# Performance work log

Hardware: AMD Instinct MI355X
Metric: run time of the kernel (lower is better)

## Reference

```python
import jax, jax.numpy as jnp
import numpy as np

GAMMA = 0.99
LMBD = 0.95  # lambda is unused in live math: in-loop advantages are overwritten by returns - values
EPS = 0.2
T, S, H, A = 262144, 128, 1024, 16


def setup_inputs() -> dict:
    key = jax.random.key(0)
    ks = jax.random.split(key, 12)
    states = jax.random.normal(ks[0], (T, S), jnp.float32)
    actions = jax.random.normal(ks[1], (T, A), jnp.float32)
    rewards = jax.random.normal(ks[2], (T, 1), jnp.float32)
    values = jax.random.normal(ks[3], (T, 1), jnp.float32)
    masks = jax.random.randint(ks[4], (T, 1), 0, 2, jnp.int32)
    W1 = jax.random.normal(ks[5], (S, H), jnp.float32) / np.sqrt(S)
    b1 = jnp.zeros((H,), jnp.float32)
    W_mu = jax.random.normal(ks[6], (H, A), jnp.float32) / np.sqrt(H)
    b_mu = jnp.zeros((A,), jnp.float32)
    W_lv = jax.random.normal(ks[7], (H, A), jnp.float32) / np.sqrt(H)
    b_lv = jnp.zeros((A,), jnp.float32)
    # beta (old policy) log-probs: computed from the same net + small noise so that
    # ratio = exp(sum(pi_logp - beta_logp)) stays numerically reasonable, as in real PPO.
    h = jnp.tanh(states @ W1 + b1)
    mu = h @ W_mu + b_mu
    std = jnp.exp(0.5 * (h @ W_lv + b_lv))
    logp = -0.5 * jnp.square((actions - mu) / std) - jnp.log(std) - 0.5 * jnp.log(2.0 * jnp.pi)
    beta_log_probs = logp + 0.01 * jax.random.normal(ks[8], (T, A), jnp.float32)
    return dict(states=states, actions=actions, rewards=rewards, values=values,
                beta_log_probs=beta_log_probs, W1=W1, b1=b1, W_mu=W_mu, b_mu=b_mu,
                W_lv=W_lv, b_lv=b_lv, masks=masks)


def reference(states, actions, rewards, values, beta_log_probs,
              W1, b1, W_mu, b_mu, W_lv, b_lv, masks):
    m = masks.astype(rewards.dtype)  # [T,1] 1=continue, 0=episode boundary

    # reversed masked discounted-return recurrence: returns[i] = r[i] + gamma * prev_return * m[i]
    def step(prev_ret, inp):
        r, mi = inp
        ret = r + GAMMA * prev_ret * mi
        return ret, ret

    _, returns = jax.lax.scan(step, jnp.zeros((1,), rewards.dtype), (rewards, m), reverse=True)
    # (deltas / in-loop GAE advantages in the source are dead code: overwritten below)
    advantages = returns - values                      # [T,1]
    a_hat = (advantages - advantages.mean()) / (advantages.std(ddof=1) + 1e-7)

    # pi(states) -> mu, logvar (value head unused here)
    h = jnp.tanh(states @ W1 + b1)                     # [T,H]
    mu = h @ W_mu + b_mu                               # [T,A]
    logvar = h @ W_lv + b_lv
    std = jnp.exp(0.5 * logvar)
    pi_log_probs = -0.5 * jnp.square((actions - mu) / std) - jnp.log(std) - 0.5 * jnp.log(2.0 * jnp.pi)

    blp = jax.lax.stop_gradient(beta_log_probs)        # .detach() in source
    ratio = jnp.exp(jnp.sum(pi_log_probs - blp, axis=1, keepdims=True))  # [T,1]

    actor_loss = -jnp.mean(jnp.minimum(ratio * a_hat,
                                       jnp.clip(ratio, 1.0 - EPS, 1.0 + EPS) * a_hat))
    critic_loss = jnp.mean(jnp.square(advantages))
    return actor_loss + critic_loss
```

## Files before the change

### kernel.cpp

```cpp
#include <hip/hip_runtime.h>
#include <math.h>


typedef __attribute__((ext_vector_type(8))) short short8_t;
typedef __attribute__((ext_vector_type(4))) short short4_t;
typedef __attribute__((ext_vector_type(4))) float float4_t;
typedef __attribute__((ext_vector_type(4))) unsigned uint4_t;

#define T_TOTAL 262144
#define S_DIM 128
#define H_DIM 1024
#define A_DIM 16
#define GAMMA 0.99f
#define SEG_LEN 64
#define NSEG 4096
#define GRP 16
#define NGRP 256

#define WS_SUM   0
#define WS_SUMSQ 1
#define WS_MEAN  2
#define WS_ISTD  3
#define WS_TERM  4
#define WS_SEGA  8
#define WS_SEGB  (WS_SEGA + NSEG)
#define WS_INC   (WS_SEGB + NSEG)
#define WS_ADV   (WS_INC + NSEG)
#define WS_W1F   (WS_ADV + T_TOTAL)
#define WS_WHF   (WS_W1F + 65536)

#define SM_SIZE 32784

__device__ __forceinline__ short f2bf(float f) {
  unsigned u = __float_as_uint(f);
  u += 0x7fffu + ((u >> 16) & 1u);
  return (short)(u >> 16);
}

__device__ __forceinline__ float fast_tanh(float x) {
  float e = __expf(2.0f * x);
  return 1.0f - __fdividef(2.0f, e + 1.0f);
}

__device__ __forceinline__ unsigned cvt_pk_bf16(float lo, float hi) {
  unsigned r;
  asm("v_cvt_pk_bf16_f32 %0, %1, %2" : "=v"(r) : "v"(lo), "v"(hi));
  return r;
}

__device__ __forceinline__ void permlane32_swap2(unsigned& a, unsigned& b) {
  asm("v_permlane32_swap_b32 %0, %1" : "+v"(a), "+v"(b));
}

__global__ void prep_all(const float* __restrict__ W1,
                         const float* __restrict__ W_mu,
                         const float* __restrict__ W_lv,
                         const float* __restrict__ rewards,
                         const int* __restrict__ masks,
                         float* __restrict__ ws,
                         short* __restrict__ w1f,
                         short* __restrict__ whf) {
  const int blk = blockIdx.x;
  if (blk < 64) {
    int id = blk * 256 + threadIdx.x;
    int lane = id & 63;
    int kf = (id >> 6) & 3;
    int nt = id >> 8;
    int quad = lane >> 4, col = nt * 16 + (lane & 15);
    int kbase = kf * 32 + quad * 8;
#pragma unroll
    for (int e = 0; e < 8; ++e)
      w1f[(size_t)id * 8 + e] = f2bf(W1[(size_t)(kbase + e) * H_DIM + col]);
  } else if (blk < 80) {
    int id = (blk - 64) * 256 + threadIdx.x;
    int lane = id & 63;
    int kf = (id >> 6) & 31;
    int nt = id >> 11;
    const float* src = nt ? W_lv : W_mu;
    int quad = lane >> 4, col = lane & 15;
    int hbase = kf * 32 + ((quad >> 1) << 4) + ((quad & 1) << 2);
#pragma unroll
    for (int e = 0; e < 8; ++e) {
      int hh = hbase + ((e >> 2) << 3) + (e & 3);
      whf[(size_t)id * 8 + e] = f2bf(src[(size_t)hh * A_DIM + col]);
    }
  } else if (blk < 96) {
    int g = (blk - 80) * 256 + threadIdx.x;
    int lo = g * SEG_LEN;
    const float4* r4 = (const float4*)(rewards + lo);
    const int4* m4 = (const int4*)(masks + lo);
    float a = 1.0f, b = 0.0f;
#pragma unroll 4
    for (int c = 15; c >= 0; --c) {
      float4 r = r4[c]; int4 mm = m4[c];
      float gi;
      gi = GAMMA * (float)mm.w; b = r.w + gi * b; a = gi * a;
      gi = GAMMA * (float)mm.z; b = r.z + gi * b; a = gi * a;
      gi = GAMMA * (float)mm.y; b = r.y + gi * b; a = gi * a;
      gi = GAMMA * (float)mm.x; b = r.x + gi * b; a = gi * a;
    }
    ws[WS_SEGA + g] = a;
    ws[WS_SEGB + g] = b;
  } else {
    if (threadIdx.x < 8) ws[threadIdx.x] = 0.0f;
  }
}

__global__ void scan_pass2(float* __restrict__ ws) {
  __shared__ float gA[NGRP], gB[NGRP], ginc[NGRP];
  int t = threadIdx.x;
  int lo = t * GRP, hi = lo + GRP - 1;
  float A = 1.0f, B = 0.0f;
  for (int s = hi; s >= lo; --s) {
    float as = ws[WS_SEGA + s], bs = ws[WS_SEGB + s];
    B = bs + as * B;
    A = as * A;
  }
  gA[t] = A; gB[t] = B;
  __syncthreads();
  if (t == 0) {
    float x = 0.0f;
    ginc[NGRP - 1] = 0.0f;
    for (int g = NGRP - 1; g >= 1; --g) {
      x = gB[g] + gA[g] * x;
      ginc[g - 1] = x;
    }
  }
  __syncthreads();
  float x = ginc[t];
  for (int s = hi; s >= lo; --s) {
    ws[WS_INC + s] = x;
    x = ws[WS_SEGB + s] + ws[WS_SEGA + s] * x;
  }
}

__global__ void scan_pass3(const float* __restrict__ rewards,
                           const int* __restrict__ masks,
                           const float* __restrict__ values,
                           float* __restrict__ ws) {
  int g = blockIdx.x * blockDim.x + threadIdx.x;
  int lo = g * SEG_LEN;
  float x = ws[WS_INC + g];
  const float4* r4 = (const float4*)(rewards + lo);
  const int4* m4 = (const int4*)(masks + lo);
  const float4* v4 = (const float4*)(values + lo);
  float4* adv4 = (float4*)(ws + WS_ADV + lo);
  float s1 = 0.0f, s2 = 0.0f;
#pragma unroll 4
  for (int c = 15; c >= 0; --c) {
    float4 r = r4[c]; int4 mm = m4[c]; float4 v = v4[c];
    float gi;
    gi = GAMMA * (float)mm.w; x = r.w + gi * x; float aw = x - v.w;
    gi = GAMMA * (float)mm.z; x = r.z + gi * x; float az = x - v.z;
    gi = GAMMA * (float)mm.y; x = r.y + gi * x; float ay = x - v.y;
    gi = GAMMA * (float)mm.x; x = r.x + gi * x; float ax = x - v.x;
    float4 o; o.x = ax; o.y = ay; o.z = az; o.w = aw;
    adv4[c] = o;
    s1 += ax + ay + az + aw;
    s2 += ax * ax + ay * ay + az * az + aw * aw;
  }
  for (int m = 1; m < 64; m <<= 1) {
    s1 += __shfl_xor(s1, m);
    s2 += __shfl_xor(s2, m);
  }
  if ((threadIdx.x & 63) == 0) {
    atomicAdd(&ws[WS_SUM], s1);
    atomicAdd(&ws[WS_SUMSQ], s2);
  }
}

__launch_bounds__(256, 2)
__global__ void main2(const float* __restrict__ states,
                      const float* __restrict__ actions,
                      const float* __restrict__ beta,
                      const float* __restrict__ b1g,
                      const float* __restrict__ bmug,
                      const float* __restrict__ blvg,
                      const short* __restrict__ W1f,
                      const short* __restrict__ Whf,
                      float* __restrict__ ws) {
  __shared__ __align__(16) unsigned char smem[SM_SIZE];
  short* Ab = (short*)smem;

  const int tid = threadIdx.x;
  const int lane = tid & 63;
  const int w = tid >> 6;
  const int quad = lane >> 4;
  const int t0 = blockIdx.x * 64;

  {
    const float4* src = (const float4*)(states + (size_t)t0 * S_DIM);
#pragma unroll
    for (int i = 0; i < 8; ++i) {
      int f = tid + i * 256;
      float4 v = src[f];
      int row = f >> 5, kq = f & 31;
      int rt = row >> 4, rr = row & 15;
      int k = kq * 4, kf = k >> 5, qd = (k >> 3) & 3, j0 = k & 7;
      short4_t pk;
      pk[0] = f2bf(v.x); pk[1] = f2bf(v.y); pk[2] = f2bf(v.z); pk[3] = f2bf(v.w);
      *(short4_t*)(Ab + (((rt * 4 + kf) * 64 + qd * 16 + rr) << 3) + j0) = pk;
    }
  }
  __syncthreads();

  short8_t sfrag[4][4];
#pragma unroll
  for (int rt = 0; rt < 4; ++rt)
#pragma unroll
    for (int kf = 0; kf < 4; ++kf)
      sfrag[rt][kf] = *((const short8_t*)Ab + (rt * 4 + kf) * 64 + lane);

  float4_t acc2[4][2];
#pragma unroll
  for (int rt = 0; rt < 4; ++rt) {
    acc2[rt][0] = (float4_t){0.f, 0.f, 0.f, 0.f};
    acc2[rt][1] = (float4_t){0.f, 0.f, 0.f, 0.f};
  }

  for (int kk = 0; kk < 8; ++kk) {
    const int nt1 = w * 16 + kk * 2;
    const short8_t* w1p = (const short8_t*)W1f + nt1 * 256 + lane;
    short8_t wf0[4], wf1[4];
#pragma unroll
    for (int kf = 0; kf < 4; ++kf) {
      wf0[kf] = w1p[kf * 64];
      wf1[kf] = w1p[256 + kf * 64];
    }
    const float4 b1a = *(const float4*)(b1g + nt1 * 16 + quad * 4);
    const float4 b1b = *(const float4*)(b1g + nt1 * 16 + 16 + quad * 4);
    const int kf2 = w * 8 + kk;
    const short8_t* whp = (const short8_t*)Whf + kf2 * 64 + lane;
    const short8_t wmu = whp[0];
    const short8_t wlv = whp[2048];
#pragma unroll
    for (int rt = 0; rt < 4; ++rt) {
      float4_t c0 = (float4_t){b1a.x, b1a.y, b1a.z, b1a.w};
      float4_t c1 = (float4_t){b1b.x, b1b.y, b1b.z, b1b.w};
#pragma unroll
      for (int kf = 0; kf < 4; ++kf) {
        c0 = __builtin_amdgcn_mfma_f32_16x16x32_bf16(wf0[kf], sfrag[rt][kf], c0, 0, 0, 0);
        c1 = __builtin_amdgcn_mfma_f32_16x16x32_bf16(wf1[kf], sfrag[rt][kf], c1, 0, 0, 0);
      }
      unsigned p00 = cvt_pk_bf16(fast_tanh(c0[0]), fast_tanh(c0[1]));
      unsigned p01 = cvt_pk_bf16(fast_tanh(c0[2]), fast_tanh(c0[3]));
      unsigned p10 = cvt_pk_bf16(fast_tanh(c1[0]), fast_tanh(c1[1]));
      unsigned p11 = cvt_pk_bf16(fast_tanh(c1[2]), fast_tanh(c1[3]));
      permlane32_swap2(p00, p10);
      permlane32_swap2(p01, p11);
      uint4_t u = (uint4_t){p00, p01, p10, p11};
      short8_t b2 = __builtin_bit_cast(short8_t, u);
      acc2[rt][0] = __builtin_amdgcn_mfma_f32_16x16x32_bf16(wmu, b2, acc2[rt][0], 0, 0, 0);
      acc2[rt][1] = __builtin_amdgcn_mfma_f32_16x16x32_bf16(wlv, b2, acc2[rt][1], 0, 0, 0);
    }
  }

  __syncthreads();
  float* red = (float*)smem;
  float* lds_term = (float*)(smem + 32768);
#pragma unroll
  for (int rt = 0; rt < 4; ++rt)
#pragma unroll
    for (int nt = 0; nt < 2; ++nt)
      *(float4_t*)(red + ((((w * 4 + rt) * 2 + nt) * 64 + lane) << 2)) = acc2[rt][nt];
  __syncthreads();

  const float s1 = ws[WS_SUM], s2 = ws[WS_SUMSQ];
  const float n = (float)T_TOTAL;
  const float mean = s1 / n;
  float var = (s2 - s1 * s1 / n) / (n - 1.0f);
  var = fmaxf(var, 0.0f);
  const float istd = 1.0f / (sqrtf(var) + 1e-7f);

  const int rt = w;
  const int tcol = lane & 15;
  const int t = t0 + rt * 16 + tcol;
  const float4 bmu4 = *(const float4*)(bmug + quad * 4);
  const float4 blv4 = *(const float4*)(blvg + quad * 4);
  float m0 = bmu4.x, m1 = bmu4.y, m2 = bmu4.z, m3 = bmu4.w;
  float l0 = blv4.x, l1 = blv4.y, l2 = blv4.z, l3 = blv4.w;
  const float4_t* rp = (const float4_t*)red;
#pragma unroll
  for (int wv = 0; wv < 4; ++wv) {
    float4_t mv = rp[((wv * 4 + rt) * 2 + 0) * 64 + lane];
    float4_t lvv = rp[((wv * 4 + rt) * 2 + 1) * 64 + lane];
    m0 += mv[0]; m1 += mv[1]; m2 += mv[2]; m3 += mv[3];
    l0 += lvv[0]; l1 += lvv[1]; l2 += lvv[2]; l3 += lvv[3];
  }
  const float4 av = *(const float4*)(actions + (size_t)t * A_DIM + quad * 4);
  const float4 bv = *(const float4*)(beta + (size_t)t * A_DIM + quad * 4);
  float d = 0.0f;
  {
    float isd, z;
    isd = __expf(-0.5f * l0); z = (av.x - m0) * isd;
    d += -0.5f * z * z - 0.5f * l0 - 0.9189385332046727f - bv.x;
    isd = __expf(-0.5f * l1); z = (av.y - m1) * isd;
    d += -0.5f * z * z - 0.5f * l1 - 0.9189385332046727f - bv.y;
    isd = __expf(-0.5f * l2); z = (av.z - m2) * isd;
    d += -0.5f * z * z - 0.5f * l2 - 0.9189385332046727f - bv.z;
    isd = __expf(-0.5f * l3); z = (av.w - m3) * isd;
    d += -0.5f * z * z - 0.5f * l3 - 0.9189385332046727f - bv.w;
  }
  d += __shfl_xor(d, 16);
  d += __shfl_xor(d, 32);
  float term = 0.0f;
  if (quad == 0) {
    float ratio = __expf(d);
    float ah = (ws[WS_ADV + t] - mean) * istd;
    float rc = fminf(fmaxf(ratio, 0.8f), 1.2f);
    term = fminf(ratio * ah, rc * ah);
  }
  term += __shfl_xor(term, 1);
  term += __shfl_xor(term, 2);
  term += __shfl_xor(term, 4);
  term += __shfl_xor(term, 8);
  if (lane == 0) lds_term[w] = term;
  __syncthreads();
  if (tid == 0)
    atomicAdd(&ws[WS_TERM], lds_term[0] + lds_term[1] + lds_term[2] + lds_term[3]);
}

__global__ void finalize(const float* __restrict__ ws, float* __restrict__ out) {
  if (threadIdx.x == 0) {
    float n = (float)T_TOTAL;
    out[0] = ws[WS_SUMSQ] / n - ws[WS_TERM] / n;
  }
}

extern "C" void kernel_launch(void* const* d_in, const int* in_sizes, int n_in,
                              void* d_out, int out_size, void* d_ws, size_t ws_size,
                              hipStream_t stream) {
  const float* states  = (const float*)d_in[0];
  const float* actions = (const float*)d_in[1];
  const float* rewards = (const float*)d_in[2];
  const float* values  = (const float*)d_in[3];
  const float* beta    = (const float*)d_in[4];
  const float* W1      = (const float*)d_in[5];
  const float* b1      = (const float*)d_in[6];
  const float* W_mu    = (const float*)d_in[7];
  const float* b_mu    = (const float*)d_in[8];
  const float* W_lv    = (const float*)d_in[9];
  const float* b_lv    = (const float*)d_in[10];
  const int*   masks   = (const int*)d_in[11];
  float* ws = (float*)d_ws;
  float* out = (float*)d_out;
  short* w1f = (short*)(ws + WS_W1F);
  short* whf = (short*)(ws + WS_WHF);

  hipLaunchKernelGGL(prep_all, dim3(97), dim3(256), 0, stream,
                     W1, W_mu, W_lv, rewards, masks, ws, w1f, whf);
  hipLaunchKernelGGL(scan_pass2, dim3(1), dim3(NGRP), 0, stream, ws);
  hipLaunchKernelGGL(scan_pass3, dim3(NSEG / 256), dim3(256), 0, stream,
                     rewards, masks, values, ws);
  hipLaunchKernelGGL(main2, dim3(T_TOTAL / 64), dim3(256), 0, stream,
                     states, actions, beta, b1, b_mu, b_lv, w1f, whf, ws);
  hipLaunchKernelGGL(finalize, dim3(1), dim3(64), 0, stream, ws, out);
}
```

Before: 391.5 us.

## Fuse scan passes into cooperative kernel, fold finalize, and simplify tanh

```diff
diff --git a/kernel.cpp b/kernel.cpp
--- a/kernel.cpp
+++ b/kernel.cpp
@@ -1,10 +1,14 @@
 #include <hip/hip_runtime.h>
+#include <hip/hip_cooperative_groups.h>
 #include <math.h>
 
+
+namespace cg = cooperative_groups;
 
 typedef __attribute__((ext_vector_type(8))) short short8_t;
 typedef __attribute__((ext_vector_type(4))) short short4_t;
 typedef __attribute__((ext_vector_type(4))) float float4_t;
+typedef __attribute__((ext_vector_type(2))) unsigned uint2_t;
 typedef __attribute__((ext_vector_type(4))) unsigned uint4_t;
 
 #define T_TOTAL 262144
@@ -12,20 +16,17 @@
 #define H_DIM 1024
 #define A_DIM 16
 #define GAMMA 0.99f
-#define SEG_LEN 64
-#define NSEG 4096
-#define GRP 16
-#define NGRP 256
+#define LOG2E2 2.8853900817779268f
 
 #define WS_SUM   0
 #define WS_SUMSQ 1
-#define WS_MEAN  2
-#define WS_ISTD  3
 #define WS_TERM  4
+#define WS_CNT   5
 #define WS_SEGA  8
-#define WS_SEGB  (WS_SEGA + NSEG)
-#define WS_INC   (WS_SEGB + NSEG)
-#define WS_ADV   (WS_INC + NSEG)
+#define WS_B1S   (WS_SEGA + 2048)
+#define WS_SEGB  (WS_SEGA + 4096)
+#define WS_INC   (WS_SEGB + 4096)
+#define WS_ADV   (WS_INC + 4096)
 #define WS_W1F   (WS_ADV + T_TOTAL)
 #define WS_WHF   (WS_W1F + 65536)
 
@@ -37,11 +38,6 @@
   return (short)(u >> 16);
 }
 
-__device__ __forceinline__ float fast_tanh(float x) {
-  float e = __expf(2.0f * x);
-  return 1.0f - __fdividef(2.0f, e + 1.0f);
-}
-
 __device__ __forceinline__ unsigned cvt_pk_bf16(float lo, float hi) {
   unsigned r;
   asm("v_cvt_pk_bf16_f32 %0, %1, %2" : "=v"(r) : "v"(lo), "v"(hi));
@@ -52,133 +48,156 @@
   asm("v_permlane32_swap_b32 %0, %1" : "+v"(a), "+v"(b));
 }
 
-__global__ void prep_all(const float* __restrict__ W1,
-                         const float* __restrict__ W_mu,
-                         const float* __restrict__ W_lv,
-                         const float* __restrict__ rewards,
-                         const int* __restrict__ masks,
-                         float* __restrict__ ws,
-                         short* __restrict__ w1f,
-                         short* __restrict__ whf) {
-  const int blk = blockIdx.x;
-  if (blk < 64) {
-    int id = blk * 256 + threadIdx.x;
-    int lane = id & 63;
-    int kf = (id >> 6) & 3;
-    int nt = id >> 8;
-    int quad = lane >> 4, col = nt * 16 + (lane & 15);
+__device__ __forceinline__ float tanh2(float x, float bs) {
+  float a = __builtin_fmaf(x, LOG2E2, bs);
+  float e = __builtin_amdgcn_exp2f(a);
+  float r = __builtin_amdgcn_rcpf(e + 1.0f);
+  return __builtin_fmaf(r, -2.0f, 1.0f);
+}
+
+__global__ __launch_bounds__(256, 1) void pre_coop(
+    const float* __restrict__ rewards, const int* __restrict__ masks,
+    const float* __restrict__ values, const float* __restrict__ W1,
+    const float* __restrict__ W_mu, const float* __restrict__ W_lv,
+    const float* __restrict__ b1,
+    float* __restrict__ ws, short* __restrict__ w1f, short* __restrict__ whf) {
+  cg::grid_group grid = cg::this_grid();
+  const int tid = threadIdx.x;
+  const int b = blockIdx.x;
+  const int gid = b * 256 + tid;
+  const int lane = tid & 63;
+  const int w = tid >> 6;
+  __shared__ float wA[4], wB[4], xbs, s1s[4], s2s[4];
+
+  if (b == 0 && tid < 8) atomicExch(&ws[tid], 0.0f);
+
+  const float4 r4 = ((const float4*)rewards)[gid];
+  const int4 m4i = ((const int4*)masks)[gid];
+  const float4 v4 = ((const float4*)values)[gid];
+  const float g0 = GAMMA * (float)m4i.x, g1 = GAMMA * (float)m4i.y;
+  const float g2 = GAMMA * (float)m4i.z, g3 = GAMMA * (float)m4i.w;
+  float A = g3, B = r4.w;
+  B = r4.z + g2 * B; A = g2 * A;
+  B = r4.y + g1 * B; A = g1 * A;
+  B = r4.x + g0 * B; A = g0 * A;
+  float SA = A, SB = B;
+#pragma unroll
+  for (int off = 1; off < 64; off <<= 1) {
+    float tA = __shfl_down(SA, off);
+    float tB = __shfl_down(SB, off);
+    if (lane + off < 64) { SB = SB + SA * tB; SA = SA * tA; }
+  }
+  float EA = __shfl_down(SA, 1), EB = __shfl_down(SB, 1);
+  if (lane == 63) { EA = 1.0f; EB = 0.0f; }
+  if (lane == 0) { wA[w] = SA; wB[w] = SB; }
+  __syncthreads();
+  if (tid == 0) {
+    float MA = wA[3], MB = wB[3];
+    MB = wB[2] + wA[2] * MB; MA = wA[2] * MA;
+    MB = wB[1] + wA[1] * MB; MA = wA[1] * MA;
+    MB = wB[0] + wA[0] * MB; MA = wA[0] * MA;
+    atomicExch(&ws[WS_SEGA + b], MA);
+    atomicExch(&ws[WS_SEGB + b], MB);
+  }
+
+  {
+    int id = gid >> 2, e0 = (gid & 3) * 2;
+    int ln = id & 63, kf = (id >> 6) & 3, nt = id >> 8;
+    int quad = ln >> 4, col = nt * 16 + (ln & 15);
     int kbase = kf * 32 + quad * 8;
-#pragma unroll
-    for (int e = 0; e < 8; ++e)
-      w1f[(size_t)id * 8 + e] = f2bf(W1[(size_t)(kbase + e) * H_DIM + col]);
-  } else if (blk < 80) {
-    int id = (blk - 64) * 256 + threadIdx.x;
-    int lane = id & 63;
-    int kf = (id >> 6) & 31;
-    int nt = id >> 11;
+    unsigned lo = (unsigned short)f2bf(W1[(size_t)(kbase + e0) * H_DIM + col]);
+    unsigned hi = (unsigned short)f2bf(W1[(size_t)(kbase + e0 + 1) * H_DIM + col]);
+    *(unsigned*)(w1f + (size_t)id * 8 + e0) = lo | (hi << 16);
+  }
+  if (gid < 16384) {
+    int id = gid >> 2, e0 = (gid & 3) * 2;
+    int ln = id & 63, kf = (id >> 6) & 31, nt = id >> 11;
     const float* src = nt ? W_lv : W_mu;
-    int quad = lane >> 4, col = lane & 15;
+    int quad = ln >> 4, col = ln & 15;
     int hbase = kf * 32 + ((quad >> 1) << 4) + ((quad & 1) << 2);
-#pragma unroll
-    for (int e = 0; e < 8; ++e) {
-      int hh = hbase + ((e >> 2) << 3) + (e & 3);
-      whf[(size_t)id * 8 + e] = f2bf(src[(size_t)hh * A_DIM + col]);
-    }
-  } else if (blk < 96) {
-    int g = (blk - 80) * 256 + threadIdx.x;
-    int lo = g * SEG_LEN;
-    const float4* r4 = (const float4*)(rewards + lo);
-    const int4* m4 = (const int4*)(masks + lo);
-    float a = 1.0f, b = 0.0f;
-#pragma unroll 4
-    for (int c = 15; c >= 0; --c) {
-      float4 r = r4[c]; int4 mm = m4[c];
-      float gi;
-      gi = GAMMA * (float)mm.w; b = r.w + gi * b; a = gi * a;
-      gi = GAMMA * (float)mm.z; b = r.z + gi * b; a = gi * a;
-      gi = GAMMA * (float)mm.y; b = r.y + gi * b; a = gi * a;
-      gi = GAMMA * (float)mm.x; b = r.x + gi * b; a = gi * a;
-    }
-    ws[WS_SEGA + g] = a;
-    ws[WS_SEGB + g] = b;
-  } else {
-    if (threadIdx.x < 8) ws[threadIdx.x] = 0.0f;
-  }
-}
-
-__global__ void scan_pass2(float* __restrict__ ws) {
-  __shared__ float gA[NGRP], gB[NGRP], ginc[NGRP];
-  int t = threadIdx.x;
-  int lo = t * GRP, hi = lo + GRP - 1;
-  float A = 1.0f, B = 0.0f;
-  for (int s = hi; s >= lo; --s) {
-    float as = ws[WS_SEGA + s], bs = ws[WS_SEGB + s];
-    B = bs + as * B;
-    A = as * A;
-  }
-  gA[t] = A; gB[t] = B;
-  __syncthreads();
-  if (t == 0) {
-    float x = 0.0f;
-    ginc[NGRP - 1] = 0.0f;
-    for (int g = NGRP - 1; g >= 1; --g) {
-      x = gB[g] + gA[g] * x;
-      ginc[g - 1] = x;
-    }
-  }
-  __syncthreads();
-  float x = ginc[t];
-  for (int s = hi; s >= lo; --s) {
-    ws[WS_INC + s] = x;
-    x = ws[WS_SEGB + s] + ws[WS_SEGA + s] * x;
-  }
-}
-
-__global__ void scan_pass3(const float* __restrict__ rewards,
-                           const int* __restrict__ masks,
-                           const float* __restrict__ values,
-                           float* __restrict__ ws) {
-  int g = blockIdx.x * blockDim.x + threadIdx.x;
-  int lo = g * SEG_LEN;
-  float x = ws[WS_INC + g];
-  const float4* r4 = (const float4*)(rewards + lo);
-  const int4* m4 = (const int4*)(masks + lo);
-  const float4* v4 = (const float4*)(values + lo);
-  float4* adv4 = (float4*)(ws + WS_ADV + lo);
-  float s1 = 0.0f, s2 = 0.0f;
-#pragma unroll 4
-  for (int c = 15; c >= 0; --c) {
-    float4 r = r4[c]; int4 mm = m4[c]; float4 v = v4[c];
-    float gi;
-    gi = GAMMA * (float)mm.w; x = r.w + gi * x; float aw = x - v.w;
-    gi = GAMMA * (float)mm.z; x = r.z + gi * x; float az = x - v.z;
-    gi = GAMMA * (float)mm.y; x = r.y + gi * x; float ay = x - v.y;
-    gi = GAMMA * (float)mm.x; x = r.x + gi * x; float ax = x - v.x;
-    float4 o; o.x = ax; o.y = ay; o.z = az; o.w = aw;
-    adv4[c] = o;
-    s1 += ax + ay + az + aw;
-    s2 += ax * ax + ay * ay + az * az + aw * aw;
-  }
+    int h0 = hbase + ((e0 >> 2) << 3) + (e0 & 3);
+    int h1 = hbase + (((e0 + 1) >> 2) << 3) + ((e0 + 1) & 3);
+    unsigned lo = (unsigned short)f2bf(src[(size_t)h0 * A_DIM + col]);
+    unsigned hi = (unsigned short)f2bf(src[(size_t)h1 * A_DIM + col]);
+    *(unsigned*)(whf + (size_t)id * 8 + e0) = lo | (hi << 16);
+  }
+  if (gid < 1024) ws[WS_B1S + gid] = LOG2E2 * b1[gid];
+
+  grid.sync();
+
+  if (b == 0 && w == 0) {
+    float a0 = atomicAdd(&ws[WS_SEGA + lane * 4 + 0], 0.0f);
+    float a1 = atomicAdd(&ws[WS_SEGA + lane * 4 + 1], 0.0f);
+    float a2 = atomicAdd(&ws[WS_SEGA + lane * 4 + 2], 0.0f);
+    float a3 = atomicAdd(&ws[WS_SEGA + lane * 4 + 3], 0.0f);
+    float b0 = atomicAdd(&ws[WS_SEGB + lane * 4 + 0], 0.0f);
+    float b1v = atomicAdd(&ws[WS_SEGB + lane * 4 + 1], 0.0f);
+    float b2v = atomicAdd(&ws[WS_SEGB + lane * 4 + 2], 0.0f);
+    float b3v = atomicAdd(&ws[WS_SEGB + lane * 4 + 3], 0.0f);
+    float CA = a3, CB = b3v;
+    CB = b2v + a2 * CB; CA = a2 * CA;
+    CB = b1v + a1 * CB; CA = a1 * CA;
+    CB = b0 + a0 * CB; CA = a0 * CA;
+    float PSA = CA, PSB = CB;
+#pragma unroll
+    for (int off = 1; off < 64; off <<= 1) {
+      float tA = __shfl_down(PSA, off);
+      float tB = __shfl_down(PSB, off);
+      if (lane + off < 64) { PSB = PSB + PSA * tB; PSA = PSA * tA; }
+    }
+    float XEA = __shfl_down(PSA, 1), XEB = __shfl_down(PSB, 1);
+    if (lane == 63) { XEA = 1.0f; XEB = 0.0f; }
+    float x = XEB;
+    atomicExch(&ws[WS_INC + lane * 4 + 3], x);
+    x = b3v + a3 * x;
+    atomicExch(&ws[WS_INC + lane * 4 + 2], x);
+    x = b2v + a2 * x;
+    atomicExch(&ws[WS_INC + lane * 4 + 1], x);
+    x = b1v + a1 * x;
+    atomicExch(&ws[WS_INC + lane * 4 + 0], x);
+  }
+
+  grid.sync();
+
+  if (tid == 0) xbs = atomicAdd(&ws[WS_INC + b], 0.0f);
+  __syncthreads();
+  float xw = xbs;
+#pragma unroll
+  for (int w2 = 3; w2 > 0; --w2)
+    if (w2 > w) xw = wB[w2] + wA[w2] * xw;
+  float x = EB + EA * xw;
+  float x3 = r4.w + g3 * x;
+  float x2 = r4.z + g2 * x3;
+  float x1 = r4.y + g1 * x2;
+  float x0 = r4.x + g0 * x1;
+  float4 adv;
+  adv.x = x0 - v4.x; adv.y = x1 - v4.y; adv.z = x2 - v4.z; adv.w = x3 - v4.w;
+  ((float4*)(ws + WS_ADV))[gid] = adv;
+  float s1 = adv.x + adv.y + adv.z + adv.w;
+  float s2 = adv.x * adv.x + adv.y * adv.y + adv.z * adv.z + adv.w * adv.w;
+#pragma unroll
   for (int m = 1; m < 64; m <<= 1) {
     s1 += __shfl_xor(s1, m);
     s2 += __shfl_xor(s2, m);
   }
-  if ((threadIdx.x & 63) == 0) {
-    atomicAdd(&ws[WS_SUM], s1);
-    atomicAdd(&ws[WS_SUMSQ], s2);
-  }
-}
-
-__launch_bounds__(256, 2)
+  if (lane == 0) { s1s[w] = s1; s2s[w] = s2; }
+  __syncthreads();
+  if (tid == 0) {
+    atomicAdd(&ws[WS_SUM], s1s[0] + s1s[1] + s1s[2] + s1s[3]);
+    atomicAdd(&ws[WS_SUMSQ], s2s[0] + s2s[1] + s2s[2] + s2s[3]);
+  }
+}
+
+__launch_bounds__(256, 3)
 __global__ void main2(const float* __restrict__ states,
                       const float* __restrict__ actions,
                       const float* __restrict__ beta,
-                      const float* __restrict__ b1g,
                       const float* __restrict__ bmug,
                       const float* __restrict__ blvg,
                       const short* __restrict__ W1f,
                       const short* __restrict__ Whf,
-                      float* __restrict__ ws) {
+                      float* __restrict__ ws,
+                      float* __restrict__ out) {
   __shared__ __align__(16) unsigned char smem[SM_SIZE];
   short* Ab = (short*)smem;
 
@@ -197,9 +216,10 @@
       int row = f >> 5, kq = f & 31;
       int rt = row >> 4, rr = row & 15;
       int k = kq * 4, kf = k >> 5, qd = (k >> 3) & 3, j0 = k & 7;
-      short4_t pk;
-      pk[0] = f2bf(v.x); pk[1] = f2bf(v.y); pk[2] = f2bf(v.z); pk[3] = f2bf(v.w);
-      *(short4_t*)(Ab + (((rt * 4 + kf) * 64 + qd * 16 + rr) << 3) + j0) = pk;
+      uint2_t pk2;
+      pk2[0] = cvt_pk_bf16(v.x, v.y);
+      pk2[1] = cvt_pk_bf16(v.z, v.w);
+      *(uint2_t*)(Ab + (((rt * 4 + kf) * 64 + qd * 16 + rr) << 3) + j0) = pk2;
     }
   }
   __syncthreads();
@@ -217,6 +237,8 @@
     acc2[rt][0] = (float4_t){0.f, 0.f, 0.f, 0.f};
     acc2[rt][1] = (float4_t){0.f, 0.f, 0.f, 0.f};
   }
+  const float4_t zz = (float4_t){0.f, 0.f, 0.f, 0.f};
+  const float* b1s = ws + WS_B1S;
 
   for (int kk = 0; kk < 8; ++kk) {
     const int nt1 = w * 16 + kk * 2;
@@ -227,25 +249,25 @@
       wf0[kf] = w1p[kf * 64];
       wf1[kf] = w1p[256 + kf * 64];
     }
-    const float4 b1a = *(const float4*)(b1g + nt1 * 16 + quad * 4);
-    const float4 b1b = *(const float4*)(b1g + nt1 * 16 + 16 + quad * 4);
+    const float4 b1a = *(const float4*)(b1s + nt1 * 16 + quad * 4);
+    const float4 b1b = *(const float4*)(b1s + nt1 * 16 + 16 + quad * 4);
     const int kf2 = w * 8 + kk;
     const short8_t* whp = (const short8_t*)Whf + kf2 * 64 + lane;
     const short8_t wmu = whp[0];
     const short8_t wlv = whp[2048];
 #pragma unroll
     for (int rt = 0; rt < 4; ++rt) {
-      float4_t c0 = (float4_t){b1a.x, b1a.y, b1a.z, b1a.w};
-      float4_t c1 = (float4_t){b1b.x, b1b.y, b1b.z, b1b.w};
+      float4_t c0 = zz;
+      float4_t c1 = zz;
 #pragma unroll
       for (int kf = 0; kf < 4; ++kf) {
         c0 = __builtin_amdgcn_mfma_f32_16x16x32_bf16(wf0[kf], sfrag[rt][kf], c0, 0, 0, 0);
         c1 = __builtin_amdgcn_mfma_f32_16x16x32_bf16(wf1[kf], sfrag[rt][kf], c1, 0, 0, 0);
       }
-      unsigned p00 = cvt_pk_bf16(fast_tanh(c0[0]), fast_tanh(c0[1]));
-      unsigned p01 = cvt_pk_bf16(fast_tanh(c0[2]), fast_tanh(c0[3]));
-      unsigned p10 = cvt_pk_bf16(fast_tanh(c1[0]), fast_tanh(c1[1]));
-      unsigned p11 = cvt_pk_bf16(fast_tanh(c1[2]), fast_tanh(c1[3]));
+      unsigned p00 = cvt_pk_bf16(tanh2(c0[0], b1a.x), tanh2(c0[1], b1a.y));
+      unsigned p01 = cvt_pk_bf16(tanh2(c0[2], b1a.z), tanh2(c0[3], b1a.w));
+      unsigned p10 = cvt_pk_bf16(tanh2(c1[0], b1b.x), tanh2(c1[1], b1b.y));
+      unsigned p11 = cvt_pk_bf16(tanh2(c1[2], b1b.z), tanh2(c1[3], b1b.w));
       permlane32_swap2(p00, p10);
       permlane32_swap2(p01, p11);
       uint4_t u = (uint4_t){p00, p01, p10, p11};
@@ -316,14 +338,14 @@
   term += __shfl_xor(term, 8);
   if (lane == 0) lds_term[w] = term;
   __syncthreads();
-  if (tid == 0)
+  if (tid == 0) {
     atomicAdd(&ws[WS_TERM], lds_term[0] + lds_term[1] + lds_term[2] + lds_term[3]);
-}
-
-__global__ void finalize(const float* __restrict__ ws, float* __restrict__ out) {
-  if (threadIdx.x == 0) {
-    float n = (float)T_TOTAL;
-    out[0] = ws[WS_SUMSQ] / n - ws[WS_TERM] / n;
+    __threadfence();
+    unsigned old = atomicAdd((unsigned*)ws + WS_CNT, 1u);
+    if (old == (unsigned)(gridDim.x - 1)) {
+      float termv = atomicAdd(&ws[WS_TERM], 0.0f);
+      out[0] = ws[WS_SUMSQ] / n - termv / n;
+    }
   }
 }
 
@@ -347,12 +369,10 @@
   short* w1f = (short*)(ws + WS_W1F);
   short* whf = (short*)(ws + WS_WHF);
 
-  hipLaunchKernelGGL(prep_all, dim3(97), dim3(256), 0, stream,
-                     W1, W_mu, W_lv, rewards, masks, ws, w1f, whf);
-  hipLaunchKernelGGL(scan_pass2, dim3(1), dim3(NGRP), 0, stream, ws);
-  hipLaunchKernelGGL(scan_pass3, dim3(NSEG / 256), dim3(256), 0, stream,
-                     rewards, masks, values, ws);
+  void* args[] = {(void*)&rewards, (void*)&masks, (void*)&values,
+                  (void*)&W1, (void*)&W_mu, (void*)&W_lv, (void*)&b1,
+                  (void*)&ws, (void*)&w1f, (void*)&whf};
+  hipLaunchCooperativeKernel((void*)pre_coop, dim3(256), dim3(256), args, 0, stream);
   hipLaunchKernelGGL(main2, dim3(T_TOTAL / 64), dim3(256), 0, stream,
-                     states, actions, beta, b1, b_mu, b_lv, w1f, whf, ws);
-  hipLaunchKernelGGL(finalize, dim3(1), dim3(64), 0, stream, ws, out);
-}
+                     states, actions, beta, b_mu, b_lv, w1f, whf, ws, out);
+}
```

Measured after the change: 525.0 us. 34.1% more time.
